# Kernel optimization log

Measured on AMD Instinct MI355X. Metric: run time of the kernel, lower is better.

Reference implementation:

```python
import jax, jax.numpy as jnp
import numpy as np

B, S, H = 2, 2048, 2048
NH, NKV, HD = 16, 4, 128
GROUPS = NH // NKV
THETA = 10000.0
EPS = 1e-6


def setup_inputs() -> dict:
    key = jax.random.key(0)
    ks = jax.random.split(key, 6)
    scale = 0.02
    return {
        "hidden_states": jax.random.normal(ks[0], (B, S, H), jnp.float32),
        "wq": jax.random.normal(ks[1], (NH * HD, H), jnp.float32) * scale,
        "wk": jax.random.normal(ks[2], (NKV * HD, H), jnp.float32) * scale,
        "wv": jax.random.normal(ks[3], (NKV * HD, H), jnp.float32) * scale,
        "wo": jax.random.normal(ks[4], (H, NH * HD), jnp.float32) * scale,
        "q_norm_weight": jnp.ones((HD,), jnp.float32),
        "k_norm_weight": jnp.ones((HD,), jnp.float32),
    }


def _rope_tables(seq_len):
    inv_freq = 1.0 / (THETA ** (jnp.arange(0, HD, 2, dtype=jnp.float32) / HD))
    t = jnp.arange(seq_len, dtype=jnp.float32)
    freqs = jnp.outer(t, inv_freq)              # [S, HD/2]
    emb = jnp.concatenate([freqs, freqs], -1)   # [S, HD]
    return jnp.cos(emb), jnp.sin(emb)


def _rotate_half(x):
    x1, x2 = x[..., : HD // 2], x[..., HD // 2:]
    return jnp.concatenate([-x2, x1], -1)


def _rmsnorm(x, w):
    var = jnp.mean(jnp.square(x), axis=-1, keepdims=True)
    return x * jax.lax.rsqrt(var + EPS) * w


def reference(hidden_states, wq, wk, wv, wo, q_norm_weight, k_norm_weight):
    b, s, _ = hidden_states.shape
    q = (hidden_states @ wq.T).reshape(b, s, NH, HD).transpose(0, 2, 1, 3)    # [b,nh,s,d]
    k = (hidden_states @ wk.T).reshape(b, s, NKV, HD).transpose(0, 2, 1, 3)   # [b,nkv,s,d]
    v = (hidden_states @ wv.T).reshape(b, s, NKV, HD).transpose(0, 2, 1, 3)

    cos, sin = _rope_tables(s)                  # [s,d]
    q = q * cos + _rotate_half(q) * sin
    k = k * cos + _rotate_half(k) * sin

    # fused QK RMSNorm (applied inside fused_qknorm_flash_attention)
    q = _rmsnorm(q, q_norm_weight)
    k = _rmsnorm(k, k_norm_weight)

    # GQA: share each kv head across GROUPS query heads without materializing repeats
    qg = q.reshape(b, NKV, GROUPS, s, HD)
    scale = 1.0 / jnp.sqrt(jnp.float32(HD))
    scores = jnp.einsum('bhgqd,bhkd->bhgqk', qg, k) * scale   # [b,nkv,g,s,s]
    causal = jnp.tril(jnp.ones((s, s), bool))
    scores = jnp.where(causal, scores, jnp.finfo(scores.dtype).min)
    probs = jax.nn.softmax(scores, axis=-1)
    out = jnp.einsum('bhgqk,bhkd->bhgqd', probs, v)            # [b,nkv,g,s,d]
    out = out.reshape(b, NH, s, HD).transpose(0, 2, 1, 3).reshape(b, s, NH * HD)
    return out @ wo.T
```

## Files before the change

### kernel.cpp

```cpp
#include <hip/hip_runtime.h>
#include <math.h>

typedef __bf16 bf16;
typedef __bf16 bf16x8 __attribute__((ext_vector_type(8)));
typedef __bf16 bf16x4 __attribute__((ext_vector_type(4)));
typedef float f32x4 __attribute__((ext_vector_type(4)));

#define B_DIM 2
#define S_LEN 2048
#define H_DIM 2048
#define NH 16
#define NKV 4
#define HD 128

__device__ __forceinline__ void gl_lds16(const void* g, void* l) {
    __builtin_amdgcn_global_load_lds(
        (const __attribute__((address_space(1))) unsigned int*)g,
        (__attribute__((address_space(3))) unsigned int*)l, 16, 0, 0);
}

__global__ __launch_bounds__(256) void cast_all(const float* __restrict__ s0,
                                                const float* __restrict__ s1,
                                                const float* __restrict__ s2,
                                                const float* __restrict__ s3,
                                                const float* __restrict__ s4,
                                                bf16* __restrict__ dst) {
    const int i = blockIdx.x * 256 + threadIdx.x;
    const float* src;
    int off;
    if (i < 2097152)      { src = s0; off = 0; }
    else if (i < 3145728) { src = s1; off = 2097152; }
    else if (i < 3407872) { src = s2; off = 3145728; }
    else if (i < 3670016) { src = s3; off = 3407872; }
    else                  { src = s4; off = 3670016; }
    float4 f = ((const float4*)src)[i - off];
    bf16x4 o = { (bf16)f.x, (bf16)f.y, (bf16)f.z, (bf16)f.w };
    *(bf16x4*)(dst + (size_t)i * 4) = o;
}

template <typename OutT>
__global__ __launch_bounds__(256) void gemm_bt(const bf16* __restrict__ A,
                                               const bf16* __restrict__ Bt,
                                               OutT* __restrict__ C,
                                               int M, int N, int K) {
    __shared__ __align__(16) bf16 As[128 * 32];
    __shared__ __align__(16) bf16 Bs[128 * 32];
    const int t = threadIdx.x;
    const int lane = t & 63, w = t >> 6;
    const int wm = (w & 1) * 64, wn = (w >> 1) * 64;
    const int lr = lane & 15, quad = lane >> 4;
    const int m0 = blockIdx.x * 128, n0 = blockIdx.y * 128;
    const int lrow = lane >> 2, lk = (lane & 3) * 8;
    f32x4 acc[4][4];
#pragma unroll
    for (int i = 0; i < 4; i++)
#pragma unroll
        for (int j = 0; j < 4; j++) acc[i][j] = (f32x4){0.f, 0.f, 0.f, 0.f};

    for (int k0 = 0; k0 < K; k0 += 32) {
        __syncthreads();
#pragma unroll
        for (int i = 0; i < 2; i++) {
            const int r0 = i * 64 + w * 16;
            gl_lds16(A + (size_t)(m0 + r0 + lrow) * K + k0 + lk, &As[r0 * 32]);
            gl_lds16(Bt + (size_t)(n0 + r0 + lrow) * K + k0 + lk, &Bs[r0 * 32]);
        }
        __syncthreads();
        bf16x8 af[4], bfr[4];
#pragma unroll
        for (int i = 0; i < 4; i++) af[i] = *(const bf16x8*)&As[(wm + i * 16 + lr) * 32 + quad * 8];
#pragma unroll
        for (int j = 0; j < 4; j++) bfr[j] = *(const bf16x8*)&Bs[(wn + j * 16 + lr) * 32 + quad * 8];
#pragma unroll
        for (int i = 0; i < 4; i++)
#pragma unroll
            for (int j = 0; j < 4; j++)
                acc[i][j] = __builtin_amdgcn_mfma_f32_16x16x32_bf16(af[i], bfr[j], acc[i][j], 0, 0, 0);
    }
#pragma unroll
    for (int i = 0; i < 4; i++) {
        int m = m0 + wm + i * 16 + quad * 4;
#pragma unroll
        for (int j = 0; j < 4; j++) {
            int n = n0 + wn + j * 16 + lr;
#pragma unroll
            for (int r = 0; r < 4; r++)
                C[(size_t)(m + r) * N + n] = (OutT)acc[i][j][r];
        }
    }
}

__global__ __launch_bounds__(256) void rope_rms(const bf16* __restrict__ qkv,
                                                const float* __restrict__ qw,
                                                const float* __restrict__ kw,
                                                bf16* __restrict__ qb,
                                                bf16* __restrict__ kb,
                                                bf16* __restrict__ vt) {
    const int tok = blockIdx.x;
    const int b = tok >> 11, s = tok & (S_LEN - 1);
    const int lane = threadIdx.x & 63, w = threadIdx.x >> 6;
    const bf16* row = qkv + (size_t)tok * 3072;
    const float inv = expf(-(float)lane * (9.210340371976184f / 64.f));
    const float ang = (float)s * inv;
    float s_, c_;
    sincosf(ang, &s_, &c_);
    const float wq1 = qw[lane], wq2 = qw[lane + 64];
    const float wk1 = kw[lane], wk2 = kw[lane + 64];
    for (int u = w; u < 24; u += 4) {
        if (u < 16) {
            const float x1 = (float)row[u * 128 + lane], x2 = (float)row[u * 128 + 64 + lane];
            float y1 = x1 * c_ - x2 * s_;
            float y2 = x2 * c_ + x1 * s_;
            float ss = y1 * y1 + y2 * y2;
#pragma unroll
            for (int m = 1; m < 64; m <<= 1) ss += __shfl_xor(ss, m);
            const float r = rsqrtf(ss * (1.f / 128.f) + 1e-6f);
            size_t o = ((size_t)(b * NH + u) * S_LEN + s) * HD;
            qb[o + lane]      = (bf16)(y1 * r * wq1);
            qb[o + 64 + lane] = (bf16)(y2 * r * wq2);
        } else if (u < 20) {
            const int kh = u - 16;
            const float x1 = (float)row[2048 + kh * 128 + lane], x2 = (float)row[2048 + kh * 128 + 64 + lane];
            float y1 = x1 * c_ - x2 * s_;
            float y2 = x2 * c_ + x1 * s_;
            float ss = y1 * y1 + y2 * y2;
#pragma unroll
            for (int m = 1; m < 64; m <<= 1) ss += __shfl_xor(ss, m);
            const float r = rsqrtf(ss * (1.f / 128.f) + 1e-6f);
            size_t base = (size_t)(b * NKV + kh) * 16 * 16384;
            kb[base + (size_t)(lane >> 3) * 16384 + s * 8 + (lane & 7)]       = (bf16)(y1 * r * wk1);
            kb[base + (size_t)(8 + (lane >> 3)) * 16384 + s * 8 + (lane & 7)] = (bf16)(y2 * r * wk2);
        } else {
            const int vh = u - 20;
            const float x1 = (float)row[2560 + vh * 128 + lane], x2 = (float)row[2560 + vh * 128 + 64 + lane];
            size_t base = ((size_t)(b * NKV + vh) * 256 + (s >> 3)) * 1024 + (s & 7);
            vt[base + (size_t)lane * 8]        = (bf16)x1;
            vt[base + (size_t)(lane + 64) * 8] = (bf16)x2;
        }
    }
}

__global__ __launch_bounds__(256, 2) void flash(const bf16* __restrict__ qg,
                                                const bf16* __restrict__ kg,
                                                const bf16* __restrict__ vg,
                                                bf16* __restrict__ attn) {
    const int idx = blockIdx.x;
    const int g = idx >> 5;
    const int qt = (g < 8) ? (15 - g) : (g - 8);
    const int hb = idx & 31;
    const int h = hb & 15, b = hb >> 4;
    const int kvh = h >> 2;
    const bf16* qh = qg + (size_t)(b * NH + h) * S_LEN * HD;
    const bf16* kh = kg + (size_t)(b * NKV + kvh) * (16 * 16384);
    const bf16* vh = vg + (size_t)(b * NKV + kvh) * (256 * 1024);
    __shared__ __align__(16) bf16 Ks[16 * 512];
    __shared__ __align__(16) bf16 Vs[8 * 1152];
    __shared__ __align__(16) bf16 Ps[4][32 * 72];
    const int t = threadIdx.x, lane = t & 63, w = t >> 6, lr = lane & 15, quad = lane >> 4;
    bf16* psw = Ps[w];
    if (t < 128) {
        const bf16 one = (bf16)1.0f;
        bf16x8 one8 = {one, one, one, one, one, one, one, one};
        *(bf16x8*)&Vs[(t >> 4) * 1152 + 1024 + (t & 15) * 8] = one8;
    }
    const int row0 = qt * 128 + w * 32;
    bf16x8 qf[2][4];
#pragma unroll
    for (int mg = 0; mg < 2; mg++)
#pragma unroll
        for (int c = 0; c < 4; c++)
            qf[mg][c] = *(const bf16x8*)(qh + (size_t)(row0 + mg * 16 + lr) * HD + c * 32 + quad * 8);
    f32x4 o[2][8];
    f32x4 lacc[2];
#pragma unroll
    for (int mg = 0; mg < 2; mg++) {
        lacc[mg] = (f32x4){0.f, 0.f, 0.f, 0.f};
#pragma unroll
        for (int j = 0; j < 8; j++) o[mg][j] = (f32x4){0.f, 0.f, 0.f, 0.f};
    }
    const float C1 = 0.12751744f;
    const float C2 = -17.3123405f;
    const int ntile = 2 * qt + 2;

    for (int kt = 0; kt < ntile; ++kt) {
        const int kbase = kt * 64;
        __syncthreads();
#pragma unroll
        for (int i = 0; i < 4; i++) {
            const int dc = w * 4 + i;
            gl_lds16(kh + (size_t)dc * 16384 + (size_t)kbase * 8 + lane * 8, &Ks[dc * 512]);
        }
#pragma unroll
        for (int i = 0; i < 2; i++) {
            const int c = w * 2 + i;
            const bf16* src = vh + ((size_t)(kbase >> 3) + c) * 1024 + lane * 8;
            gl_lds16(src, &Vs[c * 1152]);
            gl_lds16(src + 512, &Vs[c * 1152 + 512]);
        }
        __syncthreads();
        f32x4 sacc[2][4];
#pragma unroll
        for (int mg = 0; mg < 2; mg++)
#pragma unroll
            for (int n = 0; n < 4; n++) sacc[mg][n] = (f32x4){0.f, 0.f, 0.f, 0.f};
#pragma unroll
        for (int n = 0; n < 4; n++)
#pragma unroll
            for (int c = 0; c < 4; c++) {
                bf16x8 kf = *(const bf16x8*)&Ks[(c * 4 + quad) * 512 + (n * 16 + lr) * 8];
                sacc[0][n] = __builtin_amdgcn_mfma_f32_16x16x32_bf16(qf[0][c], kf, sacc[0][n], 0, 0, 0);
                sacc[1][n] = __builtin_amdgcn_mfma_f32_16x16x32_bf16(qf[1][c], kf, sacc[1][n], 0, 0, 0);
            }
        const bool diag = (kt >= 2 * qt);
#pragma unroll
        for (int mg = 0; mg < 2; mg++)
#pragma unroll
            for (int n = 0; n < 4; n++)
#pragma unroll
                for (int r = 0; r < 4; r++) {
                    float e = exp2f(fmaf(sacc[mg][n][r], C1, C2));
                    if (diag) {
                        const int key = kbase + n * 16 + lr;
                        const int qrow = row0 + mg * 16 + quad * 4 + r;
                        e = (key <= qrow) ? e : 0.f;
                    }
                    psw[(mg * 16 + quad * 4 + r) * 72 + n * 16 + lr] = (bf16)e;
                }
        bf16x8 pf[2][2];
#pragma unroll
        for (int mg = 0; mg < 2; mg++)
#pragma unroll
            for (int k2 = 0; k2 < 2; k2++)
                pf[mg][k2] = *(const bf16x8*)&psw[(mg * 16 + lr) * 72 + k2 * 32 + quad * 8];
#pragma unroll
        for (int k2 = 0; k2 < 2; k2++) {
#pragma unroll
            for (int j = 0; j < 8; j++) {
                bf16x8 vf = *(const bf16x8*)&Vs[(k2 * 4 + quad) * 1152 + (j * 16 + lr) * 8];
                o[0][j] = __builtin_amdgcn_mfma_f32_16x16x32_bf16(pf[0][k2], vf, o[0][j], 0, 0, 0);
                o[1][j] = __builtin_amdgcn_mfma_f32_16x16x32_bf16(pf[1][k2], vf, o[1][j], 0, 0, 0);
            }
            bf16x8 vone = *(const bf16x8*)&Vs[(k2 * 4 + quad) * 1152 + (128 + lr) * 8];
            lacc[0] = __builtin_amdgcn_mfma_f32_16x16x32_bf16(pf[0][k2], vone, lacc[0], 0, 0, 0);
            lacc[1] = __builtin_amdgcn_mfma_f32_16x16x32_bf16(pf[1][k2], vone, lacc[1], 0, 0, 0);
        }
    }
#pragma unroll
    for (int mg = 0; mg < 2; mg++) {
        float inv[4];
#pragma unroll
        for (int r = 0; r < 4; r++) inv[r] = 1.0f / lacc[mg][r];
#pragma unroll
        for (int j = 0; j < 8; j++)
#pragma unroll
            for (int r = 0; r < 4; r++) {
                const int qrow = row0 + mg * 16 + quad * 4 + r;
                attn[((size_t)(b * S_LEN) + qrow) * (NH * HD) + h * HD + j * 16 + lr] =
                    (bf16)(o[mg][j][r] * inv[r]);
            }
    }
}

extern "C" void kernel_launch(void* const* d_in, const int* in_sizes, int n_in,
                              void* d_out, int out_size, void* d_ws, size_t ws_size,
                              hipStream_t stream) {
    (void)in_sizes; (void)n_in; (void)out_size; (void)ws_size;
    const float* hs  = (const float*)d_in[0];
    const float* wq  = (const float*)d_in[1];
    const float* wk  = (const float*)d_in[2];
    const float* wv  = (const float*)d_in[3];
    const float* wo  = (const float*)d_in[4];
    const float* qnw = (const float*)d_in[5];
    const float* knw = (const float*)d_in[6];
    float* out = (float*)d_out;

    char* ws = (char*)d_ws;
    size_t off = 0;
    auto alloc = [&](size_t bytes) {
        void* p = ws + off;
        off += (bytes + 255) & ~(size_t)255;
        return p;
    };
    bf16* hs_bf   = (bf16*)alloc((size_t)4096 * 2048 * 2);
    bf16* wqkv_bf = (bf16*)alloc((size_t)3072 * 2048 * 2);
    bf16* wo_bf   = (bf16*)alloc((size_t)2048 * 2048 * 2);
    bf16* qkv_bf  = (bf16*)alloc((size_t)4096 * 3072 * 2);
    bf16* q_bf    = (bf16*)alloc((size_t)B_DIM * NH * S_LEN * HD * 2);
    bf16* k_bf    = (bf16*)alloc((size_t)B_DIM * NKV * S_LEN * HD * 2);
    bf16* vt_bf   = (bf16*)alloc((size_t)B_DIM * NKV * S_LEN * HD * 2);
    bf16* at_bf   = (bf16*)alloc((size_t)4096 * 2048 * 2);

    cast_all<<<18432, 256, 0, stream>>>(hs, wq, wk, wv, wo, hs_bf);
    gemm_bt<bf16><<<dim3(32, 24), 256, 0, stream>>>(hs_bf, wqkv_bf, qkv_bf, 4096, 3072, 2048);
    rope_rms<<<4096, 256, 0, stream>>>(qkv_bf, qnw, knw, q_bf, k_bf, vt_bf);
    flash<<<dim3(512), 256, 0, stream>>>(q_bf, k_bf, vt_bf, at_bf);
    gemm_bt<float><<<dim3(32, 16), 256, 0, stream>>>(at_bf, wo_bf, out, 4096, 2048, 2048);
}
```

Baseline: 352.4 us.

## Double-buffer K/V tiles and keep P in registers via transposed MFMA

The flash kernel now stages the next K/V tile into a second LDS buffer while computing the current one, replacing the two barriers per tile with one. The QK and PV MFMAs swap operand order so the score tile comes out transposed, which lets the exponentiated P be packed straight into MFMA operand registers instead of going through an LDS round trip. V is written in a permuted key order to match, the row-sum uses a constant ones vector, and output stores become 4-wide vectors. This trades more LDS for the second buffer, which may affect occupancy, and relies on the key permutation being exactly consistent between the producer and consumer kernels.

```diff
diff --git a/kernel.cpp b/kernel.cpp
--- a/kernel.cpp
+++ b/kernel.cpp
@@ -133,7 +133,10 @@
         } else {
             const int vh = u - 20;
             const float x1 = (float)row[2560 + vh * 128 + lane], x2 = (float)row[2560 + vh * 128 + 64 + lane];
-            size_t base = ((size_t)(b * NKV + vh) * 256 + (s >> 3)) * 1024 + (s & 7);
+            const int m = s & 31;
+            const int gi = (s >> 5) * 4 + ((m & 15) >> 2);
+            const int el = ((m >> 4) << 2) | (m & 3);
+            size_t base = ((size_t)(b * NKV + vh) * 256 + gi) * 1024 + el;
             vt[base + (size_t)lane * 8]        = (bf16)x1;
             vt[base + (size_t)(lane + 64) * 8] = (bf16)x2;
         }
@@ -153,16 +156,9 @@
     const bf16* qh = qg + (size_t)(b * NH + h) * S_LEN * HD;
     const bf16* kh = kg + (size_t)(b * NKV + kvh) * (16 * 16384);
     const bf16* vh = vg + (size_t)(b * NKV + kvh) * (256 * 1024);
-    __shared__ __align__(16) bf16 Ks[16 * 512];
-    __shared__ __align__(16) bf16 Vs[8 * 1152];
-    __shared__ __align__(16) bf16 Ps[4][32 * 72];
+    __shared__ __align__(16) bf16 Ks[2][16 * 512];
+    __shared__ __align__(16) bf16 Vs[2][8 * 1024];
     const int t = threadIdx.x, lane = t & 63, w = t >> 6, lr = lane & 15, quad = lane >> 4;
-    bf16* psw = Ps[w];
-    if (t < 128) {
-        const bf16 one = (bf16)1.0f;
-        bf16x8 one8 = {one, one, one, one, one, one, one, one};
-        *(bf16x8*)&Vs[(t >> 4) * 1152 + 1024 + (t & 15) * 8] = one8;
-    }
     const int row0 = qt * 128 + w * 32;
     bf16x8 qf[2][4];
 #pragma unroll
@@ -178,26 +174,35 @@
 #pragma unroll
         for (int j = 0; j < 8; j++) o[mg][j] = (f32x4){0.f, 0.f, 0.f, 0.f};
     }
+    const bf16 one = (bf16)1.0f;
+    const bf16x8 ones8 = {one, one, one, one, one, one, one, one};
     const float C1 = 0.12751744f;
     const float C2 = -17.3123405f;
     const int ntile = 2 * qt + 2;
 
+    auto stage = [&](int kt_, int bi) {
+        const int kb = kt_ * 64;
+#pragma unroll
+        for (int i = 0; i < 4; i++) {
+            const int dc = w * 4 + i;
+            gl_lds16(kh + (size_t)dc * 16384 + (size_t)kb * 8 + lane * 8, &Ks[bi][dc * 512]);
+        }
+#pragma unroll
+        for (int i = 0; i < 2; i++) {
+            const int c = w * 2 + i;
+            const bf16* src = vh + (size_t)(8 * kt_ + ((c >> 2) << 2) + (c & 3)) * 1024 + lane * 8;
+            gl_lds16(src, &Vs[bi][c * 1024]);
+            gl_lds16(src + 512, &Vs[bi][c * 1024 + 512]);
+        }
+    };
+
+    stage(0, 0);
+    __syncthreads();
+    int cur = 0;
+
     for (int kt = 0; kt < ntile; ++kt) {
         const int kbase = kt * 64;
-        __syncthreads();
-#pragma unroll
-        for (int i = 0; i < 4; i++) {
-            const int dc = w * 4 + i;
-            gl_lds16(kh + (size_t)dc * 16384 + (size_t)kbase * 8 + lane * 8, &Ks[dc * 512]);
-        }
-#pragma unroll
-        for (int i = 0; i < 2; i++) {
-            const int c = w * 2 + i;
-            const bf16* src = vh + ((size_t)(kbase >> 3) + c) * 1024 + lane * 8;
-            gl_lds16(src, &Vs[c * 1152]);
-            gl_lds16(src + 512, &Vs[c * 1152 + 512]);
-        }
-        __syncthreads();
+        if (kt + 1 < ntile) stage(kt + 1, cur ^ 1);
         f32x4 sacc[2][4];
 #pragma unroll
         for (int mg = 0; mg < 2; mg++)
@@ -207,57 +212,52 @@
         for (int n = 0; n < 4; n++)
 #pragma unroll
             for (int c = 0; c < 4; c++) {
-                bf16x8 kf = *(const bf16x8*)&Ks[(c * 4 + quad) * 512 + (n * 16 + lr) * 8];
-                sacc[0][n] = __builtin_amdgcn_mfma_f32_16x16x32_bf16(qf[0][c], kf, sacc[0][n], 0, 0, 0);
-                sacc[1][n] = __builtin_amdgcn_mfma_f32_16x16x32_bf16(qf[1][c], kf, sacc[1][n], 0, 0, 0);
+                bf16x8 kf = *(const bf16x8*)&Ks[cur][(c * 4 + quad) * 512 + (n * 16 + lr) * 8];
+                sacc[0][n] = __builtin_amdgcn_mfma_f32_16x16x32_bf16(kf, qf[0][c], sacc[0][n], 0, 0, 0);
+                sacc[1][n] = __builtin_amdgcn_mfma_f32_16x16x32_bf16(kf, qf[1][c], sacc[1][n], 0, 0, 0);
             }
         const bool diag = (kt >= 2 * qt);
-#pragma unroll
-        for (int mg = 0; mg < 2; mg++)
+        bf16x8 pT[2][2];
+#pragma unroll
+        for (int mg = 0; mg < 2; mg++) {
+            const int qrow = row0 + mg * 16 + lr;
 #pragma unroll
             for (int n = 0; n < 4; n++)
 #pragma unroll
                 for (int r = 0; r < 4; r++) {
-                    float e = exp2f(fmaf(sacc[mg][n][r], C1, C2));
+                    float ev = exp2f(fmaf(sacc[mg][n][r], C1, C2));
                     if (diag) {
-                        const int key = kbase + n * 16 + lr;
-                        const int qrow = row0 + mg * 16 + quad * 4 + r;
-                        e = (key <= qrow) ? e : 0.f;
+                        const int key = kbase + n * 16 + quad * 4 + r;
+                        ev = (key <= qrow) ? ev : 0.f;
                     }
-                    psw[(mg * 16 + quad * 4 + r) * 72 + n * 16 + lr] = (bf16)e;
+                    pT[mg][n >> 1][(n & 1) * 4 + r] = (bf16)ev;
                 }
-        bf16x8 pf[2][2];
-#pragma unroll
-        for (int mg = 0; mg < 2; mg++)
-#pragma unroll
-            for (int k2 = 0; k2 < 2; k2++)
-                pf[mg][k2] = *(const bf16x8*)&psw[(mg * 16 + lr) * 72 + k2 * 32 + quad * 8];
+        }
 #pragma unroll
         for (int k2 = 0; k2 < 2; k2++) {
 #pragma unroll
             for (int j = 0; j < 8; j++) {
-                bf16x8 vf = *(const bf16x8*)&Vs[(k2 * 4 + quad) * 1152 + (j * 16 + lr) * 8];
-                o[0][j] = __builtin_amdgcn_mfma_f32_16x16x32_bf16(pf[0][k2], vf, o[0][j], 0, 0, 0);
-                o[1][j] = __builtin_amdgcn_mfma_f32_16x16x32_bf16(pf[1][k2], vf, o[1][j], 0, 0, 0);
+                bf16x8 vf = *(const bf16x8*)&Vs[cur][(k2 * 4 + quad) * 1024 + (j * 16 + lr) * 8];
+                o[0][j] = __builtin_amdgcn_mfma_f32_16x16x32_bf16(vf, pT[0][k2], o[0][j], 0, 0, 0);
+                o[1][j] = __builtin_amdgcn_mfma_f32_16x16x32_bf16(vf, pT[1][k2], o[1][j], 0, 0, 0);
             }
-            bf16x8 vone = *(const bf16x8*)&Vs[(k2 * 4 + quad) * 1152 + (128 + lr) * 8];
-            lacc[0] = __builtin_amdgcn_mfma_f32_16x16x32_bf16(pf[0][k2], vone, lacc[0], 0, 0, 0);
-            lacc[1] = __builtin_amdgcn_mfma_f32_16x16x32_bf16(pf[1][k2], vone, lacc[1], 0, 0, 0);
-        }
+            lacc[0] = __builtin_amdgcn_mfma_f32_16x16x32_bf16(ones8, pT[0][k2], lacc[0], 0, 0, 0);
+            lacc[1] = __builtin_amdgcn_mfma_f32_16x16x32_bf16(ones8, pT[1][k2], lacc[1], 0, 0, 0);
+        }
+        __syncthreads();
+        cur ^= 1;
     }
 #pragma unroll
     for (int mg = 0; mg < 2; mg++) {
-        float inv[4];
-#pragma unroll
-        for (int r = 0; r < 4; r++) inv[r] = 1.0f / lacc[mg][r];
-#pragma unroll
-        for (int j = 0; j < 8; j++)
-#pragma unroll
-            for (int r = 0; r < 4; r++) {
-                const int qrow = row0 + mg * 16 + quad * 4 + r;
-                attn[((size_t)(b * S_LEN) + qrow) * (NH * HD) + h * HD + j * 16 + lr] =
-                    (bf16)(o[mg][j][r] * inv[r]);
-            }
+        const float inv = 1.0f / lacc[mg][0];
+        const int qrow = row0 + mg * 16 + lr;
+        bf16* dst = attn + ((size_t)(b * S_LEN) + qrow) * (NH * HD) + h * HD + quad * 4;
+#pragma unroll
+        for (int j = 0; j < 8; j++) {
+            bf16x4 st = { (bf16)(o[mg][j][0] * inv), (bf16)(o[mg][j][1] * inv),
+                          (bf16)(o[mg][j][2] * inv), (bf16)(o[mg][j][3] * inv) };
+            *(bf16x4*)(dst + j * 16) = st;
+        }
     }
 }
 
```

Result: faster. 325.3 us (-7.7%).
